# Kernel optimization log

Hardware: AMD Instinct MI355X
Metric: run time of the kernel (lower is better)

Reference implementation:

```python
import math
import jax, jax.numpy as jnp
import numpy as np

V, D, H, L, FH = 32000, 384, 6, 6, 1536
B, S = 38, 256
HD = D // H


def setup_inputs() -> dict:
    key = jax.random.key(0)
    ks = jax.random.split(key, 16)
    sc = 0.02
    inp = {
        "x": jax.random.randint(ks[0], (B, S), 1, V, dtype=jnp.int32),
        "targets": jax.random.randint(ks[1], (B, S), 0, V, dtype=jnp.int32),
        "emb": jax.random.normal(ks[2], (V, D), jnp.float32) * sc,
        "Wqkv": jax.random.normal(ks[3], (L, 3 * D, D), jnp.float32) * sc,
        "bqkv": jnp.zeros((L, 3 * D), jnp.float32),
        "Wo": jax.random.normal(ks[4], (L, D, D), jnp.float32) * sc,
        "bo": jnp.zeros((L, D), jnp.float32),
        "gamma1": jnp.ones((L, D), jnp.float32),
        "beta1": jnp.zeros((L, D), jnp.float32),
        "W1": jax.random.normal(ks[5], (L, FH, D), jnp.float32) * sc,
        "b1": jnp.zeros((L, FH), jnp.float32),
        "W2": jax.random.normal(ks[6], (L, D, FH), jnp.float32) * sc,
        "b2": jnp.zeros((L, D), jnp.float32),
        "gamma2": jnp.ones((L, D), jnp.float32),
        "beta2": jnp.zeros((L, D), jnp.float32),
        "Wout": jax.random.normal(ks[7], (V, D), jnp.float32) * sc,
        "bout": jnp.zeros((V,), jnp.float32),
    }
    return inp


def _pos_encoding(seq_len, d_model):
    even_i = jnp.arange(0, d_model, 2, dtype=jnp.float32)
    denom = jnp.power(10000.0, even_i / d_model)  # (D/2,)
    pos = jnp.arange(seq_len, dtype=jnp.float32)[:, None]  # (S,1)
    even_pe = jnp.sin(pos / denom)
    odd_pe = jnp.cos(pos / denom)
    return jnp.stack([even_pe, odd_pe], axis=2).reshape(seq_len, d_model)


def _layer_norm(x, gamma, beta, eps=1e-5):
    mean = x.mean(axis=-1, keepdims=True)
    var = ((x - mean) ** 2).mean(axis=-1, keepdims=True)
    return gamma * (x - mean) / jnp.sqrt(var + eps) + beta


def _build_mask(x_ids, seq_len):
    # replicate the data-dependent pad mask: take the row with most non-pad
    # tokens, count its leading non-zeros -> max_length
    pad = (x_ids != 0)
    idx = jnp.argmax(pad.sum(axis=1))
    row = x_ids[idx]
    has_zero = jnp.any(row == 0)
    max_len = jnp.where(has_zero, jnp.argmax(row == 0), seq_len)
    i = jnp.arange(seq_len)[:, None]
    j = jnp.arange(seq_len)[None, :]
    allowed = (j <= i) & ~((i >= max_len) & (j >= max_len))
    return jnp.where(allowed, 0.0, -jnp.inf).astype(jnp.float32)  # (S,S)


def _forward(x, targets, emb, Wqkv, bqkv, Wo, bo, gamma1, beta1, W1, b1,
             W2, b2, gamma2, beta2, Wout, bout):
    Bn, Sn = x.shape
    h = emb[x] * math.sqrt(D) + _pos_encoding(Sn, D)[None]  # (B,S,D)
    mask = _build_mask(x, Sn)
    inv_sqrt_dk = 1.0 / math.sqrt(HD)

    def layer(h, p):
        (Wq, bq, Wo_, bo_, g1, be1, W1_, b1_, W2_, b2_, g2, be2) = p
        qkv = h @ Wq.T + bq  # (B,S,3D)
        qkv = qkv.reshape(Bn, Sn, H, 3 * HD).transpose(0, 2, 1, 3)  # (B,H,S,3hd)
        q, k, v = jnp.split(qkv, 3, axis=-1)
        scores = jnp.einsum('bhqd,bhkd->bhqk', q, k) * inv_sqrt_dk + mask
        attn = jax.nn.softmax(scores, axis=-1)
        vals = jnp.einsum('bhqk,bhkd->bhqd', attn, v)
        vals = vals.transpose(0, 2, 1, 3).reshape(Bn, Sn, D)
        att_out = vals @ Wo_.T + bo_
        h = _layer_norm(h + att_out, g1, be1)
        ffn = jax.nn.gelu(h @ W1_.T + b1_, approximate=False) @ W2_.T + b2_
        h = _layer_norm(h + ffn, g2, be2)
        return h, None

    params = (Wqkv, bqkv, Wo, bo, gamma1, beta1, W1, b1, W2, b2, gamma2, beta2)
    h, _ = jax.lax.scan(layer, h, params)

    logits = h @ Wout.T + bout  # (B,S,V)
    logp = jax.nn.log_softmax(logits, axis=-1)
    nll = -jnp.take_along_axis(logp, targets[..., None].astype(jnp.int32), axis=-1)[..., 0]
    loss = nll.mean()
    return logits, loss


def reference(x, targets, emb, Wqkv, bqkv, Wo, bo, gamma1, beta1, W1, b1,
              W2, b2, gamma2, beta2, Wout, bout):
    return _forward(x, targets, emb, Wqkv, bqkv, Wo, bo, gamma1, beta1,
                    W1, b1, W2, b2, gamma2, beta2, Wout, bout)
```

## Files before the change

### kernel.cpp

```cpp
#include <hip/hip_runtime.h>
#include <hip/hip_bf16.h>
#include <math.h>

#define VSZ 32000
#define DSZ 384
#define HSZ 6
#define LSZ 6
#define FHSZ 1536
#define BSZ 38
#define SSZ 256
#define HDSZ 64
#define NROW (BSZ*SSZ)
#define D3 (3*DSZ)
#define NTB256 (VSZ/256)

typedef __bf16 bf16;
typedef __attribute__((ext_vector_type(8))) __bf16 bf16x8;
typedef __attribute__((ext_vector_type(4))) __bf16 bf16x4;
typedef __attribute__((ext_vector_type(4))) float f32x4;

__device__ __forceinline__ void gload16(const bf16* g, bf16* l) {
  __builtin_amdgcn_global_load_lds((const __attribute__((address_space(1))) void*)g,
                                   (__attribute__((address_space(3))) void*)l, 16, 0, 0);
}

__device__ __forceinline__ int xcd_swz(int orig, int nwg) {
  int q = nwg >> 3, r = nwg & 7;
  int xcd = orig & 7, lin = orig >> 3;
  return (xcd < r ? xcd*(q+1) : r*(q+1) + (xcd - r)*q) + lin;
}

__device__ __forceinline__ float fast_erf(float x) {
  float ax = fabsf(x);
  float t = 1.0f / fmaf(0.3275911f, ax, 1.0f);
  float p = fmaf(t, 1.061405429f, -1.453152027f);
  p = fmaf(p, t, 1.421413741f);
  p = fmaf(p, t, -0.284496736f);
  p = fmaf(p, t, 0.254829592f);
  float y = 1.0f - p*t*__expf(-ax*ax);
  return copysignf(y, x);
}

struct CvtDesc { const float* s0; bf16* d0; const float* s1; bf16* d1;
                 const float* s2; bf16* d2; const float* s3; bf16* d3;
                 const float* s4; bf16* d4; };
#define C0 663552
#define C1 884736
#define C2 1769472
#define C3 2654208
#define C4 5726208
__global__ __launch_bounds__(256) void cvt_all(CvtDesc dd) {
  int i = blockIdx.x*256 + threadIdx.x;
  int st = gridDim.x*256;
  for (; i < C4; i += st) {
    const float* s; bf16* d; int o;
    if      (i < C0) { s = dd.s0; d = dd.d0; o = i; }
    else if (i < C1) { s = dd.s1; d = dd.d1; o = i - C0; }
    else if (i < C2) { s = dd.s2; d = dd.d2; o = i - C1; }
    else if (i < C3) { s = dd.s3; d = dd.d3; o = i - C2; }
    else             { s = dd.s4; d = dd.d4; o = i - C3; }
    f32x4 v = __builtin_nontemporal_load((const f32x4*)s + o);
    bf16x4 ov = { (bf16)v[0], (bf16)v[1], (bf16)v[2], (bf16)v[3] };
    *(bf16x4*)(d + 4*(size_t)o) = ov;
  }
}

__global__ __launch_bounds__(256) void pe_k(float* __restrict__ pe) {
  const float c = 2.0f/384.0f*13.287712379549449f;
  int i = blockIdx.x*256 + threadIdx.x;
  int s = i / DSZ, d = i - s*DSZ;
  int ii = d >> 1;
  float ang = (float)s * exp2f(-(float)ii * c);
  pe[i] = (d & 1) ? cosf(ang) : sinf(ang);
}

__global__ __launch_bounds__(256) void embed_k(const int* __restrict__ x,
    const float* __restrict__ emb, const float* __restrict__ pe,
    float* __restrict__ h, bf16* __restrict__ hb) {
  const float scale = 19.595917942265423f;
  int i4 = blockIdx.x*256 + threadIdx.x;
  int st = gridDim.x*256;
  for (; i4 < NROW*(DSZ/4); i4 += st) {
    int r = i4 / (DSZ/4), c4 = (i4 - r*(DSZ/4))*4;
    int tok = x[r];
    int s = r & (SSZ-1);
    f32x4 e = *((const f32x4*)(emb + (size_t)tok*DSZ + c4));
    f32x4 p = *((const f32x4*)(pe + (size_t)s*DSZ + c4));
    f32x4 v = { e[0]*scale + p[0], e[1]*scale + p[1],
                e[2]*scale + p[2], e[3]*scale + p[3] };
    *(f32x4*)(h + (size_t)i4*4) = v;
    bf16x4 o = { (bf16)v[0], (bf16)v[1], (bf16)v[2], (bf16)v[3] };
    *(bf16x4*)(hb + (size_t)i4*4) = o;
  }
}

template<int MODE>
__global__ __launch_bounds__(256) void gemm_bt(const bf16* __restrict__ A,
    const bf16* __restrict__ Bm, const float* __restrict__ bias,
    bf16* __restrict__ Cv, int N, int K) {
  __shared__ __align__(16) bf16 As[2][128*64];
  __shared__ __align__(16) bf16 Bs[2][128*64];
  const int tid = threadIdx.x;
  const int lane = tid & 63, wid = tid >> 6;

  const int GX = gridDim.x, GY = gridDim.y;
  int orig = blockIdx.y*GX + blockIdx.x;
  int swz = xcd_swz(orig, GX*GY);
  int by = swz / GX, bx = swz - (swz/GX)*GX;

  const int wm = (wid >> 1) * 64, wn = (wid & 1) * 64;
  const int lr = lane & 15, lk = (lane >> 4) * 8;
  const int sx = (lr & 7) * 8;

  f32x4 acc[4][4];
  f32x4 zz = {0.f, 0.f, 0.f, 0.f};
#pragma unroll
  for (int m = 0; m < 4; ++m)
#pragma unroll
    for (int n = 0; n < 4; ++n) acc[m][n] = zz;

  const bf16* Ab = A + (size_t)by*128*K;
  const bf16* Bb = Bm + (size_t)bx*128*K;
  const int nk = K >> 6;

  auto STAGE = [&](int buf, int kt) {
#pragma unroll
    for (int c = 0; c < 4; ++c) {
      int chunk = c*256 + tid;
      int row = chunk >> 3, sub = chunk & 7;
      int scol = (sub ^ (row & 7)) * 8;
      gload16(Ab + (size_t)row*K + kt*64 + scol, &As[buf][chunk*8]);
      gload16(Bb + (size_t)row*K + kt*64 + scol, &Bs[buf][chunk*8]);
    }
  };

  STAGE(0, 0);
  __syncthreads();
  int cur = 0;
  for (int kt = 0; kt < nk; ++kt) {
    if (kt + 1 < nk) STAGE(cur ^ 1, kt + 1);
#pragma unroll
    for (int kk = 0; kk < 2; ++kk) {
      bf16x8 af[4], bfr[4];
#pragma unroll
      for (int m = 0; m < 4; ++m)
        af[m] = *(const bf16x8*)(&As[cur][(wm + m*16 + lr)*64 + ((kk*32 + lk) ^ sx)]);
#pragma unroll
      for (int n = 0; n < 4; ++n)
        bfr[n] = *(const bf16x8*)(&Bs[cur][(wn + n*16 + lr)*64 + ((kk*32 + lk) ^ sx)]);
#pragma unroll
      for (int m = 0; m < 4; ++m)
#pragma unroll
        for (int n = 0; n < 4; ++n)
          acc[m][n] = __builtin_amdgcn_mfma_f32_16x16x32_bf16(af[m], bfr[n], acc[m][n], 0, 0, 0);
    }
    __syncthreads();
    cur ^= 1;
  }

  float bv[4];
#pragma unroll
  for (int n = 0; n < 4; ++n) bv[n] = bias[bx*128 + wn + n*16 + lr];
  const int r0 = (lane >> 4) * 4;
#pragma unroll
  for (int m = 0; m < 4; ++m) {
#pragma unroll
    for (int r = 0; r < 4; ++r) {
      size_t row = (size_t)by*128 + wm + m*16 + r0 + r;
#pragma unroll
      for (int n = 0; n < 4; ++n) {
        float v = acc[m][n][r] + bv[n];
        size_t ci = row*(size_t)N + (size_t)(bx*128 + wn + n*16 + lr);
        if (MODE == 1) Cv[ci] = (bf16)v;
        else {
          v = 0.5f*v*(1.0f + fast_erf(v*0.70710678118654752f));
          Cv[ci] = (bf16)v;
        }
      }
    }
  }
}

template<int NS>
__global__ __launch_bounds__(256) void gemm_sk(const bf16* __restrict__ A,
    const bf16* __restrict__ Bm, const float* __restrict__ bias,
    float* __restrict__ P, int N, int K) {
  __shared__ __align__(16) bf16 As[2][128*64];
  __shared__ __align__(16) bf16 Bs[2][128*64];
  const int tid = threadIdx.x;
  const int lane = tid & 63, wid = tid >> 6;
  const int slice = blockIdx.z;
  const int Ksl = K / NS, kb = slice * Ksl;

  const int GX = gridDim.x, GY = gridDim.y;
  int orig = blockIdx.y*GX + blockIdx.x;
  int swz = xcd_swz(orig, GX*GY);
  int by = swz / GX, bx = swz - (swz/GX)*GX;

  const int wm = (wid >> 1) * 64, wn = (wid & 1) * 64;
  const int lr = lane & 15, lk = (lane >> 4) * 8;
  const int sx = (lr & 7) * 8;

  f32x4 acc[4][4];
  f32x4 zz = {0.f, 0.f, 0.f, 0.f};
#pragma unroll
  for (int m = 0; m < 4; ++m)
#pragma unroll
    for (int n = 0; n < 4; ++n) acc[m][n] = zz;

  const bf16* Ab = A + (size_t)by*128*K + kb;
  const bf16* Bb = Bm + (size_t)bx*128*K + kb;
  const int nk = Ksl >> 6;

  auto STAGE = [&](int buf, int kt) {
#pragma unroll
    for (int c = 0; c < 4; ++c) {
      int chunk = c*256 + tid;
      int row = chunk >> 3, sub = chunk & 7;
      int scol = (sub ^ (row & 7)) * 8;
      gload16(Ab + (size_t)row*K + kt*64 + scol, &As[buf][chunk*8]);
      gload16(Bb + (size_t)row*K + kt*64 + scol, &Bs[buf][chunk*8]);
    }
  };

  STAGE(0, 0);
  __syncthreads();
  int cur = 0;
  for (int kt = 0; kt < nk; ++kt) {
    if (kt + 1 < nk) STAGE(cur ^ 1, kt + 1);
#pragma unroll
    for (int kk = 0; kk < 2; ++kk) {
      bf16x8 af[4], bfr[4];
#pragma unroll
      for (int m = 0; m < 4; ++m)
        af[m] = *(const bf16x8*)(&As[cur][(wm + m*16 + lr)*64 + ((kk*32 + lk) ^ sx)]);
#pragma unroll
      for (int n = 0; n < 4; ++n)
        bfr[n] = *(const bf16x8*)(&Bs[cur][(wn + n*16 + lr)*64 + ((kk*32 + lk) ^ sx)]);
#pragma unroll
      for (int m = 0; m < 4; ++m)
#pragma unroll
        for (int n = 0; n < 4; ++n)
          acc[m][n] = __builtin_amdgcn_mfma_f32_16x16x32_bf16(af[m], bfr[n], acc[m][n], 0, 0, 0);
    }
    __syncthreads();
    cur ^= 1;
  }

  float bv[4];
#pragma unroll
  for (int n = 0; n < 4; ++n)
    bv[n] = (slice == 0) ? bias[bx*128 + wn + n*16 + lr] : 0.0f;
  const int r0 = (lane >> 4) * 4;
  float* Pw = P + (size_t)slice*NROW*N;
#pragma unroll
  for (int m = 0; m < 4; ++m) {
#pragma unroll
    for (int r = 0; r < 4; ++r) {
      size_t row = (size_t)by*128 + wm + m*16 + r0 + r;
#pragma unroll
      for (int n = 0; n < 4; ++n) {
        size_t ci = row*(size_t)N + (size_t)(bx*128 + wn + n*16 + lr);
        Pw[ci] = acc[m][n][r] + bv[n];
      }
    }
  }
}

__global__ __launch_bounds__(512, 2) void gemm256_lse(const bf16* __restrict__ A,
    const bf16* __restrict__ Bm, const float* __restrict__ bias,
    float* __restrict__ C, float* __restrict__ pmax, float* __restrict__ psum) {
  __shared__ __align__(16) bf16 As[2][256*64];
  __shared__ __align__(16) bf16 Bs[2][256*64];
  __shared__ float sm_m[4][256], sm_s[4][256];
  const int K = DSZ, N = VSZ;
  const int tid = threadIdx.x;
  const int lane = tid & 63, wid = tid >> 6;

  const int GX = gridDim.x, GY = gridDim.y;
  int orig = blockIdx.y*GX + blockIdx.x;
  int swz = xcd_swz(orig, GX*GY);
  int bx = swz / GY, by = swz - (swz/GY)*GY;

  const int wm = (wid >> 2) * 128, wn = (wid & 3) * 64;
  const int lr = lane & 15, lk = (lane >> 4) * 8;
  const int sx = (lr & 7) * 8;

  f32x4 acc[8][4];
  f32x4 zz = {0.f, 0.f, 0.f, 0.f};
#pragma unroll
  for (int m = 0; m < 8; ++m)
#pragma unroll
    for (int n = 0; n < 4; ++n) acc[m][n] = zz;

  const bf16* Ab = A + (size_t)by*256*K;
  const bf16* Bb = Bm + (size_t)bx*256*K;
  const int nk = K >> 6;

  auto STAGE = [&](int buf, int kt) {
#pragma unroll
    for (int c = 0; c < 4; ++c) {
      int chunk = c*512 + tid;
      int row = chunk >> 3, sub = chunk & 7;
      int scol = (sub ^ (row & 7)) * 8;
      gload16(Ab + (size_t)row*K + kt*64 + scol, &As[buf][chunk*8]);
      gload16(Bb + (size_t)row*K + kt*64 + scol, &Bs[buf][chunk*8]);
    }
  };

  STAGE(0, 0);
  __syncthreads();
  int cur = 0;
  for (int kt = 0; kt < nk; ++kt) {
    if (kt + 1 < nk) STAGE(cur ^ 1, kt + 1);
#pragma unroll
    for (int kk = 0; kk < 2; ++kk) {
      bf16x8 af[8], bfr[4];
#pragma unroll
      for (int n = 0; n < 4; ++n)
        bfr[n] = *(const bf16x8*)(&Bs[cur][(wn + n*16 + lr)*64 + ((kk*32 + lk) ^ sx)]);
#pragma unroll
      for (int m = 0; m < 8; ++m)
        af[m] = *(const bf16x8*)(&As[cur][(wm + m*16 + lr)*64 + ((kk*32 + lk) ^ sx)]);
#pragma unroll
      for (int m = 0; m < 8; ++m)
#pragma unroll
        for (int n = 0; n < 4; ++n)
          acc[m][n] = __builtin_amdgcn_mfma_f32_16x16x32_bf16(af[m], bfr[n], acc[m][n], 0, 0, 0);
    }
    __syncthreads();
    cur ^= 1;
  }

  float bv[4];
#pragma unroll
  for (int n = 0; n < 4; ++n) bv[n] = bias[bx*256 + wn + n*16 + lr];
  const int r0 = (lane >> 4) * 4;

#pragma unroll
  for (int m = 0; m < 8; ++m) {
#pragma unroll
    for (int r = 0; r < 4; ++r) {
      const int rl = wm + m*16 + r0 + r;
      size_t row = (size_t)by*256 + rl;
      float v0 = acc[m][0][r] + bv[0], v1 = acc[m][1][r] + bv[1];
      float v2 = acc[m][2][r] + bv[2], v3 = acc[m][3][r] + bv[3];
      size_t cb = row*(size_t)N + (size_t)(bx*256 + wn + lr);
      __builtin_nontemporal_store(v0, &C[cb]);
      __builtin_nontemporal_store(v1, &C[cb + 16]);
      __builtin_nontemporal_store(v2, &C[cb + 32]);
      __builtin_nontemporal_store(v3, &C[cb + 48]);
      float mx = fmaxf(fmaxf(v0, v1), fmaxf(v2, v3));
#pragma unroll
      for (int o = 1; o <= 8; o <<= 1) mx = fmaxf(mx, __shfl_xor(mx, o));
      float s = __expf(v0-mx) + __expf(v1-mx) + __expf(v2-mx) + __expf(v3-mx);
#pragma unroll
      for (int o = 1; o <= 8; o <<= 1) s += __shfl_xor(s, o);
      if (lr == 0) { sm_m[wid & 3][rl] = mx; sm_s[wid & 3][rl] = s; }
    }
  }
  __syncthreads();
  if (tid < 256) {
    float m = -1e30f, s = 0.f;
#pragma unroll
    for (int c = 0; c < 4; ++c) {
      float mi = sm_m[c][tid], si = sm_s[c][tid];
      float nm = fmaxf(m, mi);
      s = s*__expf(m - nm) + si*__expf(mi - nm);
      m = nm;
    }
    size_t row = (size_t)by*256 + tid;
    pmax[row*NTB256 + bx] = m;
    psum[row*NTB256 + bx] = s;
  }
}

__global__ __launch_bounds__(256) void attn_mfma(const bf16* __restrict__ qkv,
                                                 bf16* __restrict__ vals) {
  __shared__ __align__(16) ushort Ks[256*72];
  __shared__ __align__(16) ushort Vt[64*264];
  const int tid = threadIdx.x;
  const int lane = tid & 63, w = tid >> 6;
  const int lo = lane & 15, hi = lane >> 4;
  const int bid = blockIdx.x;
  const int qt = bid & 3, bh = bid >> 2;
  const int b = bh / HSZ, hh = bh - b*HSZ;
  const int nkr = (qt + 1) * 64;
  const int qb = qt*64 + w*16;
  const int ntile = qt*4 + w + 1;
  const int kkmax = (ntile + 1) >> 1;

  {
    const int jr = tid >> 3, cc = (tid & 7) * 8;
    for (int p = 0; p < (qt+1)*2; ++p) {
      int j = p*32 + jr;
      const bf16* base = qkv + ((size_t)(b*SSZ + j))*D3 + hh*192 + 64 + cc;
      uint4 kq = *(const uint4*)base;
      *(uint2*)(&Ks[j*72 + cc])     = make_uint2(kq.x, kq.y);
      *(uint2*)(&Ks[j*72 + cc + 4]) = make_uint2(kq.z, kq.w);
    }
  }
  for (int k = tid; k < nkr; k += 256) {
    const bf16* vrow = qkv + ((size_t)(b*SSZ + k))*D3 + hh*192 + 128;
#pragma unroll
    for (int c = 0; c < 8; ++c) {
      uint4 vv = *(const uint4*)(vrow + c*8);
      const ushort* u = (const ushort*)&vv;
#pragma unroll
      for (int j = 0; j < 8; ++j)
        Vt[(c*8 + j)*264 + k] = u[j];
    }
  }

  bf16x8 qf0, qf1;
  {
    const bf16* qrow = qkv + ((size_t)(b*SSZ + qb + lo))*D3 + hh*192 + hi*8;
    qf0 = *(const bf16x8*)(qrow);
    qf1 = *(const bf16x8*)(qrow + 32);
  }
  __syncthreads();

  f32x4 zz = {0.f, 0.f, 0.f, 0.f};
  f32x4 sacc[16];
#pragma unroll
  for (int n = 0; n < 16; ++n) sacc[n] = zz;
#pragma unroll
  for (int n = 0; n < 16; ++n)
    if (n < ntile) {
      const bf16* kb0 = (const bf16*)&Ks[(n*16 + lo)*72 + hi*8];
      bf16x8 bf0 = *(const bf16x8*)(kb0);
      bf16x8 bf1 = *(const bf16x8*)(kb0 + 32);
      sacc[n] = __builtin_amdgcn_mfma_f32_16x16x32_bf16(qf0, bf0, sacc[n], 0, 0, 0);
      sacc[n] = __builtin_amdgcn_mfma_f32_16x16x32_bf16(qf1, bf1, sacc[n], 0, 0, 0);
    }
  __syncthreads();

  float mrow[4] = {-1e30f, -1e30f, -1e30f, -1e30f};
#pragma unroll
  for (int n = 0; n < 16; ++n)
    if (n < ntile) {
#pragma unroll
      for (int r = 0; r < 4; ++r) {
        int kcol = n*16 + lo, qi = qb + hi*4 + r;
        float s = (kcol <= qi) ? sacc[n][r]*0.125f : -1e30f;
        sacc[n][r] = s;
        mrow[r] = fmaxf(mrow[r], s);
      }
    }
#pragma unroll
  for (int r = 0; r < 4; ++r)
#pragma unroll
    for (int o = 1; o <= 8; o <<= 1)
      mrow[r] = fmaxf(mrow[r], __shfl_xor(mrow[r], o));

  ushort* Pl = &Ks[w*64*72];
  float lsum[4] = {0.f, 0.f, 0.f, 0.f};
#pragma unroll
  for (int n = 0; n < 16; ++n)
    if (n < 2*kkmax) {
#pragma unroll
      for (int r = 0; r < 4; ++r) {
        float e = 0.f;
        if (n < ntile) { e = __expf(sacc[n][r] - mrow[r]); lsum[r] += e; }
        bf16 eb = (bf16)e;
        Pl[(hi*4 + r)*264 + n*16 + lo] = *(const ushort*)&eb;
      }
    }
#pragma unroll
  for (int r = 0; r < 4; ++r)
#pragma unroll
    for (int o = 1; o <= 8; o <<= 1)
      lsum[r] += __shfl_xor(lsum[r], o);

  asm volatile("s_waitcnt lgkmcnt(0)" ::: "memory");

  f32x4 oacc[4];
#pragma unroll
  for (int nd = 0; nd < 4; ++nd) oacc[nd] = zz;
#pragma unroll
  for (int kk = 0; kk < 8; ++kk)
    if (kk < kkmax) {
      bf16x8 pf = *(const bf16x8*)((const bf16*)&Pl[lo*264 + kk*32 + hi*8]);
#pragma unroll
      for (int nd = 0; nd < 4; ++nd) {
        bf16x8 vf = *(const bf16x8*)((const bf16*)&Vt[(nd*16 + lo)*264 + kk*32 + hi*8]);
        oacc[nd] = __builtin_amdgcn_mfma_f32_16x16x32_bf16(pf, vf, oacc[nd], 0, 0, 0);
      }
    }

#pragma unroll
  for (int r = 0; r < 4; ++r) {
    float inv = 1.0f / lsum[r];
    size_t row = (size_t)(b*SSZ + qb + hi*4 + r);
#pragma unroll
    for (int nd = 0; nd < 4; ++nd)
      vals[row*DSZ + hh*64 + nd*16 + lo] = (bf16)(oacc[nd][r] * inv);
  }
}

template<int NS>
__global__ __launch_bounds__(256) void ln_sum(const float* __restrict__ P,
    const float* __restrict__ gamma, const float* __restrict__ beta,
    float* __restrict__ h, bf16* __restrict__ hb) {
  const int t = threadIdx.x;
  const int lane = t & 63, w = t >> 6;
  const int row = blockIdx.x*4 + w;
  const size_t base = (size_t)row*DSZ;
  float v[6];
  float s = 0.f;
#pragma unroll
  for (int k = 0; k < 6; ++k) {
    int idx = lane + k*64;
    float acc = h[base + idx];
#pragma unroll
    for (int sl = 0; sl < NS; ++sl)
      acc += P[(size_t)sl*NROW*DSZ + base + idx];
    v[k] = acc;
    s += acc;
  }
#pragma unroll
  for (int o = 32; o; o >>= 1) s += __shfl_xor(s, o);
  float mean = s * (1.0f/DSZ);
  float s2 = 0.f;
#pragma unroll
  for (int k = 0; k < 6; ++k) { float dv = v[k] - mean; s2 += dv*dv; }
#pragma unroll
  for (int o = 32; o; o >>= 1) s2 += __shfl_xor(s2, o);
  float rstd = rsqrtf(s2 * (1.0f/DSZ) + 1e-5f);
#pragma unroll
  for (int k = 0; k < 6; ++k) {
    int idx = lane + k*64;
    float outv = gamma[idx]*(v[k] - mean)*rstd + beta[idx];
    h[base + idx] = outv;
    hb[base + idx] = (bf16)outv;
  }
}

__global__ __launch_bounds__(256) void loss_merge(const float* __restrict__ pmax,
    const float* __restrict__ psum, const float* __restrict__ logits,
    const int* __restrict__ tg, float* __restrict__ nll, int ntb) {
  const int t = threadIdx.x;
  const int lane = t & 63, w = t >> 6;
  const int row = blockIdx.x*4 + w;
  float m = -1e30f, s = 0.f;
  for (int i = lane; i < ntb; i += 64) {
    float mi = pmax[(size_t)row*ntb + i], si = psum[(size_t)row*ntb + i];
    float nm = fmaxf(m, mi);
    s = s*__expf(m - nm) + si*__expf(mi - nm);
    m = nm;
  }
#pragma unroll
  for (int o = 32; o; o >>= 1) {
    float mo = __shfl_xor(m, o), so = __shfl_xor(s, o);
    float nm = fmaxf(m, mo);
    s = s*__expf(m - nm) + so*__expf(mo - nm);
    m = nm;
  }
  if (lane == 0)
    nll[row] = (m + logf(s)) - logits[(size_t)row*VSZ + tg[row]];
}

__global__ __launch_bounds__(256) void loss_final(const float* __restrict__ nll,
                                                  float* __restrict__ out) {
  __shared__ float red[4];
  const int t = threadIdx.x;
  const int lane = t & 63, w = t >> 6;
  float s = 0.f;
  for (int i = t; i < NROW; i += 256) s += nll[i];
#pragma unroll
  for (int o = 32; o; o >>= 1) s += __shfl_xor(s, o);
  if (lane == 0) red[w] = s;
  __syncthreads();
  if (t == 0) out[0] = (red[0]+red[1]+red[2]+red[3]) * (1.0f/NROW);
}

extern "C" void kernel_launch(void* const* d_in, const int* in_sizes, int n_in,
                              void* d_out, int out_size, void* d_ws, size_t ws_size,
                              hipStream_t stream) {
  (void)in_sizes; (void)n_in; (void)out_size; (void)ws_size;
  const int*   x       = (const int*)  d_in[0];
  const int*   targets = (const int*)  d_in[1];
  const float* emb     = (const float*)d_in[2];
  const float* Wqkv    = (const float*)d_in[3];
  const float* bqkv    = (const float*)d_in[4];
  const float* Wo      = (const float*)d_in[5];
  const float* bo      = (const float*)d_in[6];
  const float* gamma1  = (const float*)d_in[7];
  const float* beta1   = (const float*)d_in[8];
  const float* W1      = (const float*)d_in[9];
  const float* b1      = (const float*)d_in[10];
  const float* W2      = (const float*)d_in[11];
  const float* b2      = (const float*)d_in[12];
  const float* gamma2  = (const float*)d_in[13];
  const float* beta2   = (const float*)d_in[14];
  const float* Wout    = (const float*)d_in[15];
  const float* bout    = (const float*)d_in[16];
  float* out = (float*)d_out;

  char* wp = (char*)d_ws;
  auto carve = [&](size_t bytes)->char* {
    char* p = wp; wp += (bytes + 255) & ~(size_t)255; return p;
  };
  bf16*  Wqkv_b = (bf16*) carve((size_t)LSZ*D3*DSZ*2);
  bf16*  Wo_b   = (bf16*) carve((size_t)LSZ*DSZ*DSZ*2);
  bf16*  W1_b   = (bf16*) carve((size_t)LSZ*FHSZ*DSZ*2);
  bf16*  W2_b   = (bf16*) carve((size_t)LSZ*DSZ*FHSZ*2);
  bf16*  Wout_b = (bf16*) carve((size_t)VSZ*DSZ*2);
  float* h      = (float*)carve((size_t)NROW*DSZ*4);
  bf16*  hb     = (bf16*) carve((size_t)NROW*DSZ*2);
  bf16*  qkv_b  = (bf16*) carve((size_t)NROW*D3*2);
  bf16*  vals_b = (bf16*) carve((size_t)NROW*DSZ*2);
  float* tmp    = (float*)carve((size_t)4*NROW*DSZ*4);
  bf16*  ffn1_b = (bf16*) carve((size_t)NROW*FHSZ*2);
  float* nll    = (float*)carve((size_t)NROW*4);
  float* pmax   = (float*)carve((size_t)NROW*NTB256*4);
  float* psum   = (float*)carve((size_t)NROW*NTB256*4);
  float* pe     = (float*)carve((size_t)SSZ*DSZ*4);

  CvtDesc dd = { Wqkv, Wqkv_b, Wo, Wo_b, W1, W1_b, W2, W2_b, Wout, Wout_b };
  cvt_all<<<dim3(4096), dim3(256), 0, stream>>>(dd);

  pe_k<<<dim3(SSZ*DSZ/256), dim3(256), 0, stream>>>(pe);
  embed_k<<<dim3(2048), dim3(256), 0, stream>>>(x, emb, pe, h, hb);

  for (int l = 0; l < LSZ; ++l) {
    gemm_bt<1><<<dim3(D3/128, NROW/128), dim3(256), 0, stream>>>(
        hb, Wqkv_b + (size_t)l*D3*DSZ, bqkv + l*D3, qkv_b, D3, DSZ);
    attn_mfma<<<dim3(BSZ*HSZ*4), dim3(256), 0, stream>>>(qkv_b, vals_b);
    gemm_sk<2><<<dim3(DSZ/128, NROW/128, 2), dim3(256), 0, stream>>>(
        vals_b, Wo_b + (size_t)l*DSZ*DSZ, bo + l*DSZ, tmp, DSZ, DSZ);
    ln_sum<2><<<dim3(NROW/4), dim3(256), 0, stream>>>(
        tmp, gamma1 + l*DSZ, beta1 + l*DSZ, h, hb);
    gemm_bt<2><<<dim3(FHSZ/128, NROW/128), dim3(256), 0, stream>>>(
        hb, W1_b + (size_t)l*FHSZ*DSZ, b1 + l*FHSZ, ffn1_b, FHSZ, DSZ);
    gemm_sk<4><<<dim3(DSZ/128, NROW/128, 4), dim3(256), 0, stream>>>(
        ffn1_b, W2_b + (size_t)l*DSZ*FHSZ, b2 + l*DSZ, tmp, DSZ, FHSZ);
    ln_sum<4><<<dim3(NROW/4), dim3(256), 0, stream>>>(
        tmp, gamma2 + l*DSZ, beta2 + l*DSZ, h, hb);
  }

  gemm256_lse<<<dim3(VSZ/256, NROW/256), dim3(512), 0, stream>>>(
      hb, Wout_b, bout, out, pmax, psum);
  loss_merge<<<dim3(NROW/4), dim3(256), 0, stream>>>(pmax, psum, out, targets, nll, NTB256);
  loss_final<<<dim3(1), dim3(256), 0, stream>>>(nll, out + (size_t)NROW*VSZ);
}
```

Before: 1.308 ms.

## Deepen LM-head GEMM pipeline to 4-stage K=32 buffers with vmcnt waits

Restructures the output-projection GEMM main loop from a double-buffered K=64 tile to a four-buffer ring of K=32 tiles, with three stages prefetched and explicit s_waitcnt vmcnt counts plus raw barriers instead of __syncthreads. The swizzle pattern changes to fit the 32-wide rows. The goal is to keep more global-to-LDS loads in flight and hide memory latency behind MFMA work. LDS footprint is unchanged, but correctness now depends on the hand-counted vmcnt values matching the number of outstanding loads per stage.

```diff
diff --git a/kernel.cpp b/kernel.cpp
--- a/kernel.cpp
+++ b/kernel.cpp
@@ -270,8 +270,8 @@
 __global__ __launch_bounds__(512, 2) void gemm256_lse(const bf16* __restrict__ A,
     const bf16* __restrict__ Bm, const float* __restrict__ bias,
     float* __restrict__ C, float* __restrict__ pmax, float* __restrict__ psum) {
-  __shared__ __align__(16) bf16 As[2][256*64];
-  __shared__ __align__(16) bf16 Bs[2][256*64];
+  __shared__ __align__(16) bf16 As[4][256*32];
+  __shared__ __align__(16) bf16 Bs[4][256*32];
   __shared__ float sm_m[4][256], sm_s[4][256];
   const int K = DSZ, N = VSZ;
   const int tid = threadIdx.x;
@@ -284,7 +284,6 @@
 
   const int wm = (wid >> 2) * 128, wn = (wid & 3) * 64;
   const int lr = lane & 15, lk = (lane >> 4) * 8;
-  const int sx = (lr & 7) * 8;
 
   f32x4 acc[8][4];
   f32x4 zz = {0.f, 0.f, 0.f, 0.f};
@@ -295,41 +294,45 @@
 
   const bf16* Ab = A + (size_t)by*256*K;
   const bf16* Bb = Bm + (size_t)bx*256*K;
-  const int nk = K >> 6;
+  const int nk = 12;
 
   auto STAGE = [&](int buf, int kt) {
 #pragma unroll
-    for (int c = 0; c < 4; ++c) {
+    for (int c = 0; c < 2; ++c) {
       int chunk = c*512 + tid;
-      int row = chunk >> 3, sub = chunk & 7;
-      int scol = (sub ^ (row & 7)) * 8;
-      gload16(Ab + (size_t)row*K + kt*64 + scol, &As[buf][chunk*8]);
-      gload16(Bb + (size_t)row*K + kt*64 + scol, &Bs[buf][chunk*8]);
+      int row = chunk >> 2, sub = chunk & 3;
+      int scol = (sub ^ ((row >> 1) & 3)) * 8;
+      gload16(Ab + (size_t)row*K + kt*32 + scol, &As[buf][chunk*8]);
+      gload16(Bb + (size_t)row*K + kt*32 + scol, &Bs[buf][chunk*8]);
     }
   };
 
-  STAGE(0, 0);
-  __syncthreads();
-  int cur = 0;
+  STAGE(0, 0); STAGE(1, 1); STAGE(2, 2);
   for (int kt = 0; kt < nk; ++kt) {
-    if (kt + 1 < nk) STAGE(cur ^ 1, kt + 1);
-#pragma unroll
-    for (int kk = 0; kk < 2; ++kk) {
-      bf16x8 af[8], bfr[4];
+    if (kt < nk - 2)      asm volatile("s_waitcnt vmcnt(8)" ::: "memory");
+    else if (kt == nk-2)  asm volatile("s_waitcnt vmcnt(4)" ::: "memory");
+    else                  asm volatile("s_waitcnt vmcnt(0)" ::: "memory");
+    __builtin_amdgcn_s_barrier();
+    __builtin_amdgcn_sched_barrier(0);
+    const int buf = kt & 3;
+    bf16x8 af[8], bfr[4];
+#pragma unroll
+    for (int n = 0; n < 4; ++n) {
+      int row = wn + n*16 + lr;
+      bfr[n] = *(const bf16x8*)(&Bs[buf][row*32 + (lk ^ (((row >> 1) & 3)*8))]);
+    }
+#pragma unroll
+    for (int m = 0; m < 8; ++m) {
+      int row = wm + m*16 + lr;
+      af[m] = *(const bf16x8*)(&As[buf][row*32 + (lk ^ (((row >> 1) & 3)*8))]);
+    }
+#pragma unroll
+    for (int m = 0; m < 8; ++m)
 #pragma unroll
       for (int n = 0; n < 4; ++n)
-        bfr[n] = *(const bf16x8*)(&Bs[cur][(wn + n*16 + lr)*64 + ((kk*32 + lk) ^ sx)]);
-#pragma unroll
-      for (int m = 0; m < 8; ++m)
-        af[m] = *(const bf16x8*)(&As[cur][(wm + m*16 + lr)*64 + ((kk*32 + lk) ^ sx)]);
-#pragma unroll
-      for (int m = 0; m < 8; ++m)
-#pragma unroll
-        for (int n = 0; n < 4; ++n)
-          acc[m][n] = __builtin_amdgcn_mfma_f32_16x16x32_bf16(af[m], bfr[n], acc[m][n], 0, 0, 0);
-    }
-    __syncthreads();
-    cur ^= 1;
+        acc[m][n] = __builtin_amdgcn_mfma_f32_16x16x32_bf16(af[m], bfr[n], acc[m][n], 0, 0, 0);
+    if (kt + 3 < nk) STAGE((kt + 3) & 3, kt + 3);
+    __builtin_amdgcn_s_barrier();
   }
 
   float bv[4];
```

Result: no change. 1.308 ms (-0.0%).
